# Kernel optimization log

Hardware: AMD Instinct MI355X
Metric: run time of the kernel (lower is better)

## Reference

```python
import jax, jax.numpy as jnp
import numpy as np

TOPK = 3
RAT_S = 0.05


def conv4d(x, w, bs):
    """Faithful fused version of the looped Conv4d (stride=1, padding=1, l_k=3).

    x:  (b, c_in, l, d, h, w)
    w:  (c_out, c_in, l_k, d_k, h_k, w_k)  -- w[:, :, i] is the i-th Conv3d weight
    bs: (l_k, c_out)                        -- per-i Conv3d biases
    The torch loop computes out[f] = sum_i conv3d_i(x[f + i - l_k//2]) for valid
    frame indices, which is exactly a 4D cross-correlation; the bias of conv3d_i
    is added once per VALID i, so boundary frames get fewer bias terms.
    """
    out = jax.lax.conv_general_dilated(
        x, w, window_strides=(1, 1, 1, 1), padding=[(1, 1)] * 4,
        dimension_numbers=("NCABXY", "OIABXY", "NCABXY"))
    l_i = x.shape[2]
    l_k = w.shape[2]
    f = jnp.arange(l_i)
    j = f[:, None] + jnp.arange(l_k)[None, :] - l_k // 2  # source frame per (f, i)
    valid = ((j >= 0) & (j < l_i)).astype(x.dtype)        # (l, l_k)
    bias = valid @ bs                                     # (l, c_out)
    return out + bias.T[None, :, :, None, None, None]


def zero_window(x_aff, h, w, rat_s):
    """x_aff: (b, h*w, h, w). Suppress a Gaussian window centered at each
    channel's (r, c) source location."""
    dt = x_aff.dtype
    sr = jnp.asarray(h * rat_s, dt)
    sc = jnp.asarray(w * rat_s, dt)
    ind_r = jnp.arange(h, dtype=dt)
    ind_c = jnp.arange(w, dtype=dt)
    cent_r = jnp.repeat(jnp.arange(h), w).astype(dt)  # (h*w,)
    cent_c = jnp.tile(jnp.arange(w), h).astype(dt)    # (h*w,)
    gr = jnp.exp(-((ind_r[None, :] - cent_r[:, None]) ** 2) / (2 * sr ** 2))  # (hw, h)
    gc = jnp.exp(-((ind_c[None, :] - cent_c[:, None]) ** 2) / (2 * sc ** 2))  # (hw, w)
    g = 1.0 - gr[:, :, None] * gc[:, None, :]  # (hw, h, w)
    return x_aff * g[None]


def setup_inputs() -> dict:
    key = jax.random.key(0)
    k = jax.random.split(key, 5)
    b, c, h, w = 4, 256, 32, 32
    x = jax.random.normal(k[0], (b, c, h, w), dtype=jnp.float32)
    w1 = jax.random.normal(k[1], (16, 1, 3, 3, 3, 3), dtype=jnp.float32) * 0.2
    b1 = jax.random.normal(k[2], (3, 16), dtype=jnp.float32) * 0.05
    w2 = jax.random.normal(k[3], (1, 16, 3, 3, 3, 3), dtype=jnp.float32) * 0.1
    b2 = jax.random.normal(k[4], (3, 1), dtype=jnp.float32) * 0.05
    return {"x": x, "w1": w1, "b1": b1, "w2": w2, "b2": b2}


def reference(x, w1, b1, w2, b2):
    b, c, h1, ww1 = x.shape
    n = h1 * ww1
    # F.normalize over channel dim (p=2, eps=1e-12)
    xn = x / jnp.maximum(jnp.linalg.norm(x, axis=1, keepdims=True), 1e-12)
    q = xn.transpose(0, 2, 3, 1).reshape(b, n, c)      # (b, hw, c)
    kmat = xn.reshape(b, c, n)                          # (b, c, hw)
    aff = jnp.einsum("bnc,bcm->bnm", q, kmat)          # (b, hw, hw)
    aff = zero_window(aff.reshape(b, n, h1, ww1), h1, ww1, RAT_S)
    x_fc = aff.reshape(b, 1, h1, ww1, h1, ww1)
    y = conv4d(x_fc, w1, b1)                            # (b, 16, h1, w1, h2, w2)
    y = conv4d(y, w2, b2)                               # (b, 1,  h1, w1, h2, w2)
    xc = y.reshape(b, n, h1, ww1)                       # (b, hw, h2, w2)
    # top-k values along dim=-3 (the query/channel axis)
    vals = jax.lax.top_k(xc.transpose(0, 2, 3, 1), TOPK)[0]  # (b, h2, w2, k)
    return vals.transpose(0, 3, 1, 2)                   # (b, k, h2, w2)
```

## Files before the change

kernel.cpp:

```cpp
#include <hip/hip_runtime.h>

#define HW 1024
#define CCH 256


typedef _Float16 h2v __attribute__((ext_vector_type(2)));
typedef short bf16x8 __attribute__((ext_vector_type(8)));
typedef float f32x4 __attribute__((ext_vector_type(4)));

__device__ __forceinline__ float fdot2(unsigned a, unsigned b, float c) {
#if __has_builtin(__builtin_amdgcn_fdot2)
    return __builtin_amdgcn_fdot2(__builtin_bit_cast(h2v, a),
                                  __builtin_bit_cast(h2v, b), c, false);
#else
    h2v ha = __builtin_bit_cast(h2v, a), hb = __builtin_bit_cast(h2v, b);
    return c + (float)ha.x * (float)hb.x + (float)ha.y * (float)hb.y;
#endif
}
__device__ __forceinline__ unsigned packh2(float x, float y) {
    h2v h;
    h.x = (_Float16)x;
    h.y = (_Float16)y;
    return __builtin_bit_cast(unsigned, h);
}
__device__ __forceinline__ unsigned short f2bf(float f) {
    unsigned u = __float_as_uint(f);
    u += 0x7fffu + ((u >> 16) & 1u);
    return (unsigned short)(u >> 16);
}

__global__ __launch_bounds__(256) void norm_kernel(const float* __restrict__ x,
                                                   unsigned short* __restrict__ xnT) {
    __shared__ float red[16][17];
    __shared__ float invs[16];
    int b = blockIdx.y;
    int p0 = blockIdx.x * 16;
    int cg = threadIdx.x >> 4;
    int pp = threadIdx.x & 15;
    int p = p0 + pp;
    const float* xb = x + (size_t)b * CCH * HW;
    float ss = 0.f;
#pragma unroll
    for (int i = 0; i < 16; ++i) {
        float v = xb[(size_t)(cg * 16 + i) * HW + p];
        ss += v * v;
    }
    red[cg][pp] = ss;
    __syncthreads();
    if (threadIdx.x < 16) {
        float s = 0.f;
#pragma unroll
        for (int g = 0; g < 16; ++g) s += red[g][threadIdx.x];
        invs[threadIdx.x] = 1.0f / fmaxf(sqrtf(s), 1e-12f);
    }
    __syncthreads();
    float inv = invs[pp];
    unsigned* o = (unsigned*)(xnT + ((size_t)b * HW + p) * CCH) + cg * 8;
#pragma unroll
    for (int i = 0; i < 8; ++i) {
        int c = cg * 16 + 2 * i;
        unsigned lo = f2bf(xb[(size_t)c * HW + p] * inv);
        unsigned hi = f2bf(xb[(size_t)(c + 1) * HW + p] * inv);
        o[i] = lo | (hi << 16);
    }
}

__global__ __launch_bounds__(256) void aff_kernel(const unsigned short* __restrict__ xnT,
                                                  unsigned short* __restrict__ Af16) {
    int b = blockIdx.z;
    int p0 = blockIdx.y * 64, m0 = blockIdx.x * 64;
    const unsigned short* X = xnT + (size_t)b * HW * CCH;
    int lane = threadIdx.x & 63, w = threadIdx.x >> 6;
    int pw = p0 + (w >> 1) * 32, mw = m0 + (w & 1) * 32;
    int lr = lane & 15, lg = lane >> 4;
    f32x4 acc[2][2] = {};
    for (int ks = 0; ks < 8; ++ks) {
        int kc = ks * 32 + lg * 8;
        bf16x8 a0 = *(const bf16x8*)&X[(size_t)(pw + lr) * CCH + kc];
        bf16x8 a1 = *(const bf16x8*)&X[(size_t)(pw + 16 + lr) * CCH + kc];
        bf16x8 b0 = *(const bf16x8*)&X[(size_t)(mw + lr) * CCH + kc];
        bf16x8 b1 = *(const bf16x8*)&X[(size_t)(mw + 16 + lr) * CCH + kc];
        acc[0][0] = __builtin_amdgcn_mfma_f32_16x16x32_bf16(a0, b0, acc[0][0], 0, 0, 0);
        acc[0][1] = __builtin_amdgcn_mfma_f32_16x16x32_bf16(a0, b1, acc[0][1], 0, 0, 0);
        acc[1][0] = __builtin_amdgcn_mfma_f32_16x16x32_bf16(a1, b0, acc[1][0], 0, 0, 0);
        acc[1][1] = __builtin_amdgcn_mfma_f32_16x16x32_bf16(a1, b1, acc[1][1], 0, 0, 0);
    }
#pragma unroll
    for (int pi = 0; pi < 2; ++pi)
#pragma unroll
        for (int mi = 0; mi < 2; ++mi)
#pragma unroll
            for (int r = 0; r < 4; ++r) {
                int p = pw + 16 * pi + lg * 4 + r;
                int m = mw + 16 * mi + lr;
                int dr = (m >> 5) - (p >> 5);
                int dc = (m & 31) - (p & 31);
                float gg = 1.0f - __expf(-(float)(dr * dr + dc * dc) * 0.1953125f);
                float v = acc[pi][mi][r] * gg;
                Af16[((size_t)b * HW + p) * HW + m] =
                    __builtin_bit_cast(unsigned short, (_Float16)v);
            }
}

__global__ __launch_bounds__(256) void g_kernel(const float* __restrict__ w1,
                                                const float* __restrict__ w2,
                                                float* __restrict__ G) {
    __shared__ float w1s[1296], w2s[1296];
    int tid = threadIdx.x;
    for (int i = tid; i < 1296; i += 256) { w1s[i] = w1[i]; w2s[i] = w2[i]; }
    __syncthreads();
    int idx = blockIdx.x * 256 + tid;
    if (idx < 6561) {
        int o1 = idx / 81, o2 = idx - o1 * 81;
        float s = 0.f;
#pragma unroll
        for (int ch = 0; ch < 16; ++ch) s += w1s[ch * 81 + o1] * w2s[ch * 81 + o2];
        G[idx] = s;
    }
}

__global__ __launch_bounds__(128) void wcomp_kernel(const float* __restrict__ G,
                                                    unsigned* __restrict__ Wpk) {
    __shared__ float Gs[6561];
    int cls = blockIdx.x;
    int t = threadIdx.x;
    for (int i = t; i < 6561; i += 128) Gs[i] = G[i];
    if (t < 25) Wpk[cls * 400 + t * 16 + 15] = 0u;
    __syncthreads();
    if (t >= 125) return;
    int a = t / 25, b_ = (t / 5) % 5, c = t % 5;
    int r1c = cls / 27, c1c = (cls / 9) % 3, r2c = (cls / 3) % 3, c2c = cls % 3;
    float W[5] = {};
    for (int i2 = 0; i2 < 3; ++i2) {
        if ((r1c == 0 && i2 == 0) || (r1c == 2 && i2 == 2)) continue;
        int i1 = a - i2;
        if (i1 < 0 || i1 > 2) continue;
        for (int j2 = 0; j2 < 3; ++j2) {
            if ((c1c == 0 && j2 == 0) || (c1c == 2 && j2 == 2)) continue;
            int j1 = b_ - j2;
            if (j1 < 0 || j1 > 2) continue;
            for (int u2 = 0; u2 < 3; ++u2) {
                if ((r2c == 0 && u2 == 0) || (r2c == 2 && u2 == 2)) continue;
                int u1 = c - u2;
                if (u1 < 0 || u1 > 2) continue;
                for (int v2 = 0; v2 < 3; ++v2) {
                    if ((c2c == 0 && v2 == 0) || (c2c == 2 && v2 == 2)) continue;
                    int o2 = i2 * 27 + j2 * 9 + u2 * 3 + v2;
                    int o1b = i1 * 27 + j1 * 9 + u1 * 3;
#pragma unroll
                    for (int d = 0; d < 5; ++d) {
                        int v1 = d - v2;
                        if (v1 < 0 || v1 > 2) continue;
                        W[d] += Gs[(o1b + v1) * 81 + o2];
                    }
                }
            }
        }
    }
    unsigned* o = &Wpk[cls * 400 + (a * 5 + b_) * 16 + c * 3];
    o[0] = packh2(W[0], W[1]);
    o[1] = packh2(W[2], W[3]);
    o[2] = packh2(W[4], 0.f);
}

__global__ __launch_bounds__(1024) void bt_kernel(const float* __restrict__ w2,
                                                  const float* __restrict__ b1,
                                                  const float* __restrict__ b2,
                                                  float* __restrict__ BT) {
    __shared__ float w2s[1296], b1s[48], S0[81], S1[81], S2[81];
    int t = threadIdx.x;
    for (int i = t; i < 1296; i += 1024) w2s[i] = w2[i];
    if (t < 48) b1s[t] = b1[t];
    __syncthreads();
    if (t < 81) {
        float s0 = 0.f, s1 = 0.f, s2 = 0.f;
#pragma unroll
        for (int ch = 0; ch < 16; ++ch) {
            float w = w2s[ch * 81 + t];
            s0 += w * b1s[16 + ch];
            s1 += w * b1s[ch];
            s2 += w * b1s[32 + ch];
        }
        S0[t] = s0; S1[t] = s1; S2[t] = s2;
    }
    __syncthreads();
    if (t >= 864) return;
    int r1 = t / 27, c1c = (t / 9) % 3, r2c = (t / 3) % 3, c2c = t % 3;
    float s = b2[1] + (r1 >= 1 ? b2[0] : 0.f) + (r1 <= 30 ? b2[2] : 0.f);
    for (int i2 = 0; i2 < 3; ++i2) {
        int rr = r1 + i2 - 1;
        if (rr < 0 || rr > 31) continue;
        float m1 = (rr >= 1) ? 1.f : 0.f, m2 = (rr <= 30) ? 1.f : 0.f;
        for (int j2 = 0; j2 < 3; ++j2) {
            if ((c1c == 0 && j2 == 0) || (c1c == 2 && j2 == 2)) continue;
            for (int u2 = 0; u2 < 3; ++u2) {
                if ((r2c == 0 && u2 == 0) || (r2c == 2 && u2 == 2)) continue;
                for (int v2 = 0; v2 < 3; ++v2) {
                    if ((c2c == 0 && v2 == 0) || (c2c == 2 && v2 == 2)) continue;
                    int o2 = i2 * 27 + j2 * 9 + u2 * 3 + v2;
                    s += S0[o2] + m1 * S1[o2] + m2 * S2[o2];
                }
            }
        }
    }
    BT[t] = s;
}

#define HSD 66
__global__ __launch_bounds__(256) void convc_kernel(const unsigned short* __restrict__ Af16,
                                                    const unsigned* __restrict__ Wpk,
                                                    const float* __restrict__ BT,
                                                    float* __restrict__ xc) {
    __shared__ unsigned halo[4][36 * HSD];
    int tid = threadIdx.x;
    int w = tid >> 6, lane = tid & 63;
    int P = blockIdx.x * 4 + w;
    int b = blockIdx.y;
    int r1 = P >> 5, c1 = P & 31;
    int r1c = (r1 == 0) ? 0 : (r1 == 31) ? 2 : 1;
    int c1c = (c1 == 0) ? 0 : (c1 == 31) ? 2 : 1;

    const uint4* wsrc = (const uint4*)(Wpk + (size_t)((r1c * 3 + c1c) * 9 + 4) * 400);
    float bias = BT[r1 * 27 + c1c * 9 + 4];

    unsigned* myh = halo[w];
    for (int i = lane; i < 36 * HSD; i += 64) myh[i] = 0;

    int qr2 = lane & 15, qc = lane >> 4;
    int srow = lane & 31, sth = lane >> 5;
    int wbase = (srow + 2) * HSD + 8 * sth + 1;
    int idx4 = srow * 4 + sth * 2;

    const uint4* Ab4 = (const uint4*)(Af16 + (size_t)b * HW * HW);

    float acc0[8] = {}, acc1[8] = {};

    int pr0 = min(max(r1 - 2, 0), 31), pc0 = min(max(c1 - 2, 0), 31);
    uint4 pfA = Ab4[(size_t)(pr0 * 32 + pc0) * 128 + idx4];
    uint4 pfB = Ab4[(size_t)(pr0 * 32 + pc0) * 128 + idx4 + 1];

#pragma unroll 1
    for (int tp = 0; tp < 25; ++tp) {
        int tr = tp / 5, tc = tp - tr * 5;
        int apr = r1 + tr - 2, apc = c1 + tc - 2;
        bool valid = ((unsigned)apr < 32u) && ((unsigned)apc < 32u);
        uint4 curA = pfA, curB = pfB;
        if (tp < 24) {
            int t2 = tp + 1;
            int tr2 = t2 / 5, tc2 = t2 - tr2 * 5;
            int npr = min(max(r1 + tr2 - 2, 0), 31);
            int npc = min(max(c1 + tc2 - 2, 0), 31);
            pfA = Ab4[(size_t)(npr * 32 + npc) * 128 + idx4];
            pfB = Ab4[(size_t)(npr * 32 + npc) * 128 + idx4 + 1];
        }

        uint4 w4a = wsrc[tp * 4 + 0];
        uint4 w4b = wsrc[tp * 4 + 1];
        uint4 w4c = wsrc[tp * 4 + 2];
        uint4 w4d = wsrc[tp * 4 + 3];

        __syncthreads();
        if (valid) {
            unsigned* hb = &myh[wbase];
            hb[0] = curA.x; hb[1] = curA.y; hb[2] = curA.z; hb[3] = curA.w;
            hb[4] = curB.x; hb[5] = curB.y; hb[6] = curB.z; hb[7] = curB.w;
        }
        __syncthreads();
        if (!valid) continue;

        unsigned wr[16] = {w4a.x, w4a.y, w4a.z, w4a.w, w4b.x, w4b.y, w4b.z, w4b.w,
                           w4c.x, w4c.y, w4c.z, w4c.w, w4d.x, w4d.y, w4d.z, w4d.w};
        const unsigned* base = &myh[(2 * qr2) * HSD + 4 * qc];
#pragma unroll
        for (int i = 0; i < 6; ++i) {
            const unsigned* rp = base + i * HSD;
            uint2 e0 = *(const uint2*)rp;
            uint2 e1 = *(const uint2*)(rp + 2);
            uint2 e2 = *(const uint2*)(rp + 4);
            unsigned q0 = e0.x, q1 = e0.y, q2 = e1.x, q3 = e1.y, q4 = e2.x, q5 = e2.y;
            unsigned pp[12];
            pp[0] = q0;  pp[2] = q1;  pp[4] = q2;  pp[6] = q3;  pp[8] = q4;  pp[10] = q5;
            pp[1] = (q0 >> 16) | (q1 << 16);
            pp[3] = (q1 >> 16) | (q2 << 16);
            pp[5] = (q2 >> 16) | (q3 << 16);
            pp[7] = (q3 >> 16) | (q4 << 16);
            pp[9] = (q4 >> 16) | (q5 << 16);
            pp[11] = (q5 >> 16);
            if (i <= 4) {
                unsigned wa = wr[i * 3], wb_ = wr[i * 3 + 1], wc_ = wr[i * 3 + 2];
#pragma unroll
                for (int cc = 0; cc < 8; ++cc) {
                    float a = acc0[cc];
                    a = fdot2(wa, pp[cc], a);
                    a = fdot2(wb_, pp[cc + 2], a);
                    a = fdot2(wc_, pp[cc + 4], a);
                    acc0[cc] = a;
                }
            }
            if (i >= 1) {
                int u = i - 1;
                unsigned wa = wr[u * 3], wb_ = wr[u * 3 + 1], wc_ = wr[u * 3 + 2];
#pragma unroll
                for (int cc = 0; cc < 8; ++cc) {
                    float a = acc1[cc];
                    a = fdot2(wa, pp[cc], a);
                    a = fdot2(wb_, pp[cc + 2], a);
                    a = fdot2(wc_, pp[cc + 4], a);
                    acc1[cc] = a;
                }
            }
        }
    }

    float* xp = &xc[((size_t)b * HW + P) * HW];
    int o0 = (2 * qr2) * 32 + 8 * qc;
    int o1 = (2 * qr2 + 1) * 32 + 8 * qc;
    *(float4*)&xp[o0] = make_float4(acc0[0] + bias, acc0[1] + bias, acc0[2] + bias, acc0[3] + bias);
    *(float4*)&xp[o0 + 4] = make_float4(acc0[4] + bias, acc0[5] + bias, acc0[6] + bias, acc0[7] + bias);
    *(float4*)&xp[o1] = make_float4(acc1[0] + bias, acc1[1] + bias, acc1[2] + bias, acc1[3] + bias);
    *(float4*)&xp[o1 + 4] = make_float4(acc1[4] + bias, acc1[5] + bias, acc1[6] + bias, acc1[7] + bias);
}

__global__ __launch_bounds__(256) void expand_kernel(const unsigned short* __restrict__ Af16,
                                                     unsigned* __restrict__ Apad32) {
    int plane = blockIdx.x, b = blockIdx.y;
    const unsigned* src = (const unsigned*)(Af16 + ((size_t)b * HW + plane) * HW);
    unsigned* dst = Apad32 + ((size_t)b * HW + plane) * 720;
    for (int k = threadIdx.x; k < 720; k += 256) {
        int pr = k / 20, pcd = k - pr * 20;
        unsigned val = 0;
        if (pr >= 2 && pr < 34 && pcd >= 1 && pcd <= 16)
            val = src[(pr - 2) * 16 + (pcd - 1)];
        dst[k] = val;
    }
}

__global__ __launch_bounds__(128) void fix_kernel(const unsigned* __restrict__ Apad32,
                                                  const unsigned* __restrict__ Wpk,
                                                  const float* __restrict__ BT,
                                                  float* __restrict__ xc) {
    __shared__ __align__(16) unsigned wl[3600];
    __shared__ float bts[9];
    int tid = threadIdx.x;
    int P = blockIdx.x, b = blockIdx.y;
    int r1 = P >> 5, c1 = P & 31;
    int r1c = (r1 == 0) ? 0 : (r1 == 31) ? 2 : 1;
    int c1c = (c1 == 0) ? 0 : (c1 == 31) ? 2 : 1;

    const unsigned* wsrc = Wpk + (size_t)(r1c * 3 + c1c) * 3600;
    for (int i = tid; i < 3600; i += 128) wl[i] = wsrc[i];
    if (tid < 9) bts[tid] = BT[r1 * 27 + c1c * 9 + tid];

    int li = tid;
    bool act = li < 124;
    int qr, qc;
    if (li < 32) { qr = 0; qc = li; }
    else if (li < 64) { qr = 31; qc = li - 32; }
    else if (li < 94) { qr = li - 63; qc = 0; }
    else { qr = min(li, 123) - 93; qc = 31; }
    int r2c = (qr == 0) ? 0 : (qr == 31) ? 2 : 1;
    int c2c = (qc == 0) ? 0 : (qc == 31) ? 2 : 1;
    int v = r2c * 3 + c2c;
    int sh = (qc & 1) * 16;
    int sd = qc >> 1;

    __syncthreads();
    float acc = 0.f;

#pragma unroll 1
    for (int tp = 0; tp < 25; ++tp) {
        int tr = tp / 5, tc = tp - tr * 5;
        int apr = r1 + tr - 2, apc = c1 + tc - 2;
        if ((unsigned)apr >= 32u || (unsigned)apc >= 32u) continue;
        const unsigned* tpl = Apad32 + ((size_t)b * HW + apr * 32 + apc) * 720;
        const uint4* wv4 = (const uint4*)&wl[v * 400 + tp * 16];
        uint4 wa = wv4[0], wb = wv4[1], wc2 = wv4[2], wd = wv4[3];
        unsigned wr[16] = {wa.x, wa.y, wa.z, wa.w, wb.x, wb.y, wb.z, wb.w,
                           wc2.x, wc2.y, wc2.z, wc2.w, wd.x, wd.y, wd.z, wd.w};
#pragma unroll
        for (int u = 0; u < 5; ++u) {
            const unsigned* rp = tpl + (qr + u) * 20 + sd;
            unsigned d0 = rp[0], d1 = rp[1], d2 = rp[2];
            unsigned pa = __builtin_amdgcn_alignbit(d1, d0, sh);
            unsigned pb = __builtin_amdgcn_alignbit(d2, d1, sh);
            unsigned pc_ = __builtin_amdgcn_alignbit(0u, d2, sh);
            acc = fdot2(wr[u * 3 + 0], pa, acc);
            acc = fdot2(wr[u * 3 + 1], pb, acc);
            acc = fdot2(wr[u * 3 + 2], pc_, acc);
        }
    }

    if (act)
        xc[((size_t)b * HW + P) * HW + qr * 32 + qc] = acc + bts[v];
}

__device__ __forceinline__ void top3_push(float v, float& t0, float& t1, float& t2) {
    float n0 = fminf(t0, v);
    t0 = fmaxf(t0, v);
    float n1 = fminf(t1, n0);
    t1 = fmaxf(t1, n0);
    t2 = fmaxf(t2, n1);
}

__global__ __launch_bounds__(256) void topk1_kernel(const float* __restrict__ xc,
                                                    float* __restrict__ part) {
    int q = blockIdx.x * 256 + threadIdx.x;
    int pc = blockIdx.y, bi = blockIdx.z;
    float t0 = -1e30f, t1 = -1e30f, t2 = -1e30f;
    const float* xp = xc + (size_t)bi * HW * HW;
    for (int p = pc * 32; p < pc * 32 + 32; ++p)
        top3_push(xp[(size_t)p * HW + q], t0, t1, t2);
    float* pp = part + (size_t)(bi * 32 + pc) * 3 * HW;
    pp[q] = t0;
    pp[HW + q] = t1;
    pp[2 * HW + q] = t2;
}

__global__ __launch_bounds__(256) void topk2_kernel(const float* __restrict__ part,
                                                    float* __restrict__ out) {
    int q = blockIdx.x * 256 + threadIdx.x;
    int bi = blockIdx.y;
    float t0 = -1e30f, t1 = -1e30f, t2 = -1e30f;
    const float* pp = part + (size_t)bi * 96 * HW;
    for (int k = 0; k < 96; ++k) top3_push(pp[(size_t)k * HW + q], t0, t1, t2);
    float* ob = out + (size_t)bi * 3 * HW;
    ob[q] = t0;
    ob[HW + q] = t1;
    ob[2 * HW + q] = t2;
}

extern "C" void kernel_launch(void* const* d_in, const int* in_sizes, int n_in,
                              void* d_out, int out_size, void* d_ws, size_t ws_size,
                              hipStream_t stream) {
    const float* x = (const float*)d_in[0];
    const float* w1 = (const float*)d_in[1];
    const float* b1 = (const float*)d_in[2];
    const float* w2 = (const float*)d_in[3];
    const float* b2 = (const float*)d_in[4];
    float* out = (float*)d_out;
    float* ws = (float*)d_ws;

    unsigned short* xnT = (unsigned short*)ws;
    unsigned short* Af16 = (unsigned short*)(ws + 524288);
    float* xc = ws + 2621440;
    unsigned* Wpk = (unsigned*)(ws + 6815744);
    float* BT = ws + 6848512;
    float* part = ws + 6849536;
    unsigned* Apad32 = (unsigned*)(ws + 7242752);
    float* G = ws + 10191872;

    norm_kernel<<<dim3(64, 4), 256, 0, stream>>>(x, xnT);
    aff_kernel<<<dim3(16, 16, 4), 256, 0, stream>>>(xnT, Af16);
    expand_kernel<<<dim3(1024, 4), 256, 0, stream>>>(Af16, Apad32);
    g_kernel<<<26, 256, 0, stream>>>(w1, w2, G);
    wcomp_kernel<<<81, 128, 0, stream>>>(G, Wpk);
    bt_kernel<<<1, 1024, 0, stream>>>(w2, b1, b2, BT);
    convc_kernel<<<dim3(256, 4), 256, 0, stream>>>(Af16, Wpk, BT, xc);
    fix_kernel<<<dim3(1024, 4), 128, 0, stream>>>(Apad32, Wpk, BT, xc);
    topk1_kernel<<<dim3(4, 32, 4), 256, 0, stream>>>(xc, part);
    topk2_kernel<<<dim3(4, 4), 256, 0, stream>>>(part, out);
}
```

Baseline: 175.1 us.

## Fuse padded-affinity expansion into aff kernel and G computation into wcomp

The aff kernel now also writes each fp16 affinity value straight into the zero-padded plane layout that fix_kernel reads, so the separate expand kernel and its full re-read of Af16 go away. The padding is zeroed up front with a memset. The g_kernel is folded into wcomp_kernel, which recomputes the weight-product matrix in shared memory per block, saving a launch and a global round trip. convc's halo row stride shrinks from 66 to 34 and a minimum-occupancy launch bound is added. In exchange, aff's extra stores are scattered 2-byte writes, the memset adds a full-buffer write, and every wcomp block repeats the G computation.

```diff
diff --git a/kernel.cpp b/kernel.cpp
--- a/kernel.cpp
+++ b/kernel.cpp
@@ -66,7 +66,8 @@
 }
 
 __global__ __launch_bounds__(256) void aff_kernel(const unsigned short* __restrict__ xnT,
-                                                  unsigned short* __restrict__ Af16) {
+                                                  unsigned short* __restrict__ Af16,
+                                                  unsigned short* __restrict__ Apad16) {
     int b = blockIdx.z;
     int p0 = blockIdx.y * 64, m0 = blockIdx.x * 64;
     const unsigned short* X = xnT + (size_t)b * HW * CCH;
@@ -97,35 +98,29 @@
                 int dc = (m & 31) - (p & 31);
                 float gg = 1.0f - __expf(-(float)(dr * dr + dc * dc) * 0.1953125f);
                 float v = acc[pi][mi][r] * gg;
-                Af16[((size_t)b * HW + p) * HW + m] =
-                    __builtin_bit_cast(unsigned short, (_Float16)v);
+                unsigned short hv = __builtin_bit_cast(unsigned short, (_Float16)v);
+                Af16[((size_t)b * HW + p) * HW + m] = hv;
+                Apad16[(((size_t)b * HW + p) * 36 + 2 + (m >> 5)) * 40 + 2 + (m & 31)] = hv;
             }
 }
 
-__global__ __launch_bounds__(256) void g_kernel(const float* __restrict__ w1,
-                                                const float* __restrict__ w2,
-                                                float* __restrict__ G) {
-    __shared__ float w1s[1296], w2s[1296];
-    int tid = threadIdx.x;
-    for (int i = tid; i < 1296; i += 256) { w1s[i] = w1[i]; w2s[i] = w2[i]; }
-    __syncthreads();
-    int idx = blockIdx.x * 256 + tid;
-    if (idx < 6561) {
-        int o1 = idx / 81, o2 = idx - o1 * 81;
-        float s = 0.f;
-#pragma unroll
-        for (int ch = 0; ch < 16; ++ch) s += w1s[ch * 81 + o1] * w2s[ch * 81 + o2];
-        G[idx] = s;
-    }
-}
-
-__global__ __launch_bounds__(128) void wcomp_kernel(const float* __restrict__ G,
+__global__ __launch_bounds__(128) void wcomp_kernel(const float* __restrict__ w1,
+                                                    const float* __restrict__ w2,
                                                     unsigned* __restrict__ Wpk) {
     __shared__ float Gs[6561];
+    __shared__ float w1s[1296], w2s[1296];
     int cls = blockIdx.x;
     int t = threadIdx.x;
-    for (int i = t; i < 6561; i += 128) Gs[i] = G[i];
+    for (int i = t; i < 1296; i += 128) { w1s[i] = w1[i]; w2s[i] = w2[i]; }
     if (t < 25) Wpk[cls * 400 + t * 16 + 15] = 0u;
+    __syncthreads();
+    for (int i = t; i < 6561; i += 128) {
+        int o1 = i / 81, o2 = i - o1 * 81;
+        float s = 0.f;
+#pragma unroll
+        for (int ch = 0; ch < 16; ++ch) s += w1s[ch * 81 + o1] * w2s[ch * 81 + o2];
+        Gs[i] = s;
+    }
     __syncthreads();
     if (t >= 125) return;
     int a = t / 25, b_ = (t / 5) % 5, c = t % 5;
@@ -206,11 +201,11 @@
     BT[t] = s;
 }
 
-#define HSD 66
-__global__ __launch_bounds__(256) void convc_kernel(const unsigned short* __restrict__ Af16,
-                                                    const unsigned* __restrict__ Wpk,
-                                                    const float* __restrict__ BT,
-                                                    float* __restrict__ xc) {
+#define HSD 34
+__global__ __launch_bounds__(256, 8) void convc_kernel(const unsigned short* __restrict__ Af16,
+                                                       const unsigned* __restrict__ Wpk,
+                                                       const float* __restrict__ BT,
+                                                       float* __restrict__ xc) {
     __shared__ unsigned halo[4][36 * HSD];
     int tid = threadIdx.x;
     int w = tid >> 6, lane = tid & 63;
@@ -321,20 +316,6 @@
     *(float4*)&xp[o1 + 4] = make_float4(acc1[4] + bias, acc1[5] + bias, acc1[6] + bias, acc1[7] + bias);
 }
 
-__global__ __launch_bounds__(256) void expand_kernel(const unsigned short* __restrict__ Af16,
-                                                     unsigned* __restrict__ Apad32) {
-    int plane = blockIdx.x, b = blockIdx.y;
-    const unsigned* src = (const unsigned*)(Af16 + ((size_t)b * HW + plane) * HW);
-    unsigned* dst = Apad32 + ((size_t)b * HW + plane) * 720;
-    for (int k = threadIdx.x; k < 720; k += 256) {
-        int pr = k / 20, pcd = k - pr * 20;
-        unsigned val = 0;
-        if (pr >= 2 && pr < 34 && pcd >= 1 && pcd <= 16)
-            val = src[(pr - 2) * 16 + (pcd - 1)];
-        dst[k] = val;
-    }
-}
-
 __global__ __launch_bounds__(128) void fix_kernel(const unsigned* __restrict__ Apad32,
                                                   const unsigned* __restrict__ Wpk,
                                                   const float* __restrict__ BT,
@@ -447,13 +428,11 @@
     float* BT = ws + 6848512;
     float* part = ws + 6849536;
     unsigned* Apad32 = (unsigned*)(ws + 7242752);
-    float* G = ws + 10191872;
-
+
+    hipMemsetAsync(Apad32, 0, (size_t)4 * 1024 * 36 * 40 * 2, stream);
     norm_kernel<<<dim3(64, 4), 256, 0, stream>>>(x, xnT);
-    aff_kernel<<<dim3(16, 16, 4), 256, 0, stream>>>(xnT, Af16);
-    expand_kernel<<<dim3(1024, 4), 256, 0, stream>>>(Af16, Apad32);
-    g_kernel<<<26, 256, 0, stream>>>(w1, w2, G);
-    wcomp_kernel<<<81, 128, 0, stream>>>(G, Wpk);
+    aff_kernel<<<dim3(16, 16, 4), 256, 0, stream>>>(xnT, Af16, (unsigned short*)Apad32);
+    wcomp_kernel<<<81, 128, 0, stream>>>(w1, w2, Wpk);
     bt_kernel<<<1, 1024, 0, stream>>>(w2, b1, b2, BT);
     convc_kernel<<<dim3(256, 4), 256, 0, stream>>>(Af16, Wpk, BT, xc);
     fix_kernel<<<dim3(1024, 4), 128, 0, stream>>>(Apad32, Wpk, BT, xc);
```

Result: slower. 185.0 us (+5.7%).

## Split convc planes across two waves, fuse G into wcomp, stage fix tiles in LDS

Applied to the files above, without the earlier changes.

The center-region conv kernel now gives each affinity plane to two waves, each computing half the output rows with 4 columns per lane. This halves per-wave accumulators and LDS halo size and doubles the grid, with launch bounds asking for higher occupancy. The G weight-product kernel is folded into wcomp, removing one launch and a global round trip. fix_kernel now copies each padded plane into shared memory before the boundary-lane dot products, at the cost of extra barriers per tap.

```diff
diff --git a/kernel.cpp b/kernel.cpp
--- a/kernel.cpp
+++ b/kernel.cpp
@@ -102,30 +102,37 @@
             }
 }
 
-__global__ __launch_bounds__(256) void g_kernel(const float* __restrict__ w1,
-                                                const float* __restrict__ w2,
-                                                float* __restrict__ G) {
-    __shared__ float w1s[1296], w2s[1296];
-    int tid = threadIdx.x;
-    for (int i = tid; i < 1296; i += 256) { w1s[i] = w1[i]; w2s[i] = w2[i]; }
-    __syncthreads();
-    int idx = blockIdx.x * 256 + tid;
-    if (idx < 6561) {
-        int o1 = idx / 81, o2 = idx - o1 * 81;
-        float s = 0.f;
-#pragma unroll
-        for (int ch = 0; ch < 16; ++ch) s += w1s[ch * 81 + o1] * w2s[ch * 81 + o2];
-        G[idx] = s;
-    }
-}
-
-__global__ __launch_bounds__(128) void wcomp_kernel(const float* __restrict__ G,
+__global__ __launch_bounds__(256) void expand_kernel(const unsigned short* __restrict__ Af16,
+                                                     unsigned* __restrict__ Apad32) {
+    int plane = blockIdx.x, b = blockIdx.y;
+    const unsigned* src = (const unsigned*)(Af16 + ((size_t)b * HW + plane) * HW);
+    unsigned* dst = Apad32 + ((size_t)b * HW + plane) * 720;
+    for (int k = threadIdx.x; k < 720; k += 256) {
+        int pr = k / 20, pcd = k - pr * 20;
+        unsigned val = 0;
+        if (pr >= 2 && pr < 34 && pcd >= 1 && pcd <= 16)
+            val = src[(pr - 2) * 16 + (pcd - 1)];
+        dst[k] = val;
+    }
+}
+
+__global__ __launch_bounds__(128) void wcomp_kernel(const float* __restrict__ w1,
+                                                    const float* __restrict__ w2,
                                                     unsigned* __restrict__ Wpk) {
     __shared__ float Gs[6561];
+    __shared__ float w1s[1296], w2s[1296];
     int cls = blockIdx.x;
     int t = threadIdx.x;
-    for (int i = t; i < 6561; i += 128) Gs[i] = G[i];
+    for (int i = t; i < 1296; i += 128) { w1s[i] = w1[i]; w2s[i] = w2[i]; }
     if (t < 25) Wpk[cls * 400 + t * 16 + 15] = 0u;
+    __syncthreads();
+    for (int i = t; i < 6561; i += 128) {
+        int o1 = i / 81, o2 = i - o1 * 81;
+        float s = 0.f;
+#pragma unroll
+        for (int ch = 0; ch < 16; ++ch) s += w1s[ch * 81 + o1] * w2s[ch * 81 + o2];
+        Gs[i] = s;
+    }
     __syncthreads();
     if (t >= 125) return;
     int a = t / 25, b_ = (t / 5) % 5, c = t % 5;
@@ -206,15 +213,16 @@
     BT[t] = s;
 }
 
-#define HSD 66
-__global__ __launch_bounds__(256) void convc_kernel(const unsigned short* __restrict__ Af16,
-                                                    const unsigned* __restrict__ Wpk,
-                                                    const float* __restrict__ BT,
-                                                    float* __restrict__ xc) {
-    __shared__ unsigned halo[4][36 * HSD];
+#define HSD 34
+__global__ __launch_bounds__(256, 8) void convc_kernel(const unsigned short* __restrict__ Af16,
+                                                       const unsigned* __restrict__ Wpk,
+                                                       const float* __restrict__ BT,
+                                                       float* __restrict__ xc) {
+    __shared__ unsigned halo[2][36 * HSD];
     int tid = threadIdx.x;
     int w = tid >> 6, lane = tid & 63;
-    int P = blockIdx.x * 4 + w;
+    int pl = w >> 1, h = w & 1;
+    int P = blockIdx.x * 2 + pl;
     int b = blockIdx.y;
     int r1 = P >> 5, c1 = P & 31;
     int r1c = (r1 == 0) ? 0 : (r1 == 31) ? 2 : 1;
@@ -223,35 +231,35 @@
     const uint4* wsrc = (const uint4*)(Wpk + (size_t)((r1c * 3 + c1c) * 9 + 4) * 400);
     float bias = BT[r1 * 27 + c1c * 9 + 4];
 
-    unsigned* myh = halo[w];
-    for (int i = lane; i < 36 * HSD; i += 64) myh[i] = 0;
-
-    int qr2 = lane & 15, qc = lane >> 4;
-    int srow = lane & 31, sth = lane >> 5;
-    int wbase = (srow + 2) * HSD + 8 * sth + 1;
-    int idx4 = srow * 4 + sth * 2;
+    for (int i = tid; i < 2 * 36 * HSD; i += 256) ((unsigned*)halo)[i] = 0;
+    unsigned* myh = halo[pl];
+
+    int qr2 = 8 * h + (lane & 7);
+    int qc = lane >> 3;
+    int srow = lane & 31;
+    int sth2 = 2 * h + (lane >> 5);
+    int wbase = (srow + 2) * HSD + 4 * sth2 + 1;
+    int idx4 = srow * 4 + sth2;
 
     const uint4* Ab4 = (const uint4*)(Af16 + (size_t)b * HW * HW);
 
-    float acc0[8] = {}, acc1[8] = {};
+    float acc0[4] = {}, acc1[4] = {};
 
     int pr0 = min(max(r1 - 2, 0), 31), pc0 = min(max(c1 - 2, 0), 31);
-    uint4 pfA = Ab4[(size_t)(pr0 * 32 + pc0) * 128 + idx4];
-    uint4 pfB = Ab4[(size_t)(pr0 * 32 + pc0) * 128 + idx4 + 1];
+    uint4 pf = Ab4[(size_t)(pr0 * 32 + pc0) * 128 + idx4];
 
 #pragma unroll 1
     for (int tp = 0; tp < 25; ++tp) {
         int tr = tp / 5, tc = tp - tr * 5;
         int apr = r1 + tr - 2, apc = c1 + tc - 2;
         bool valid = ((unsigned)apr < 32u) && ((unsigned)apc < 32u);
-        uint4 curA = pfA, curB = pfB;
+        uint4 cur = pf;
         if (tp < 24) {
             int t2 = tp + 1;
             int tr2 = t2 / 5, tc2 = t2 - tr2 * 5;
             int npr = min(max(r1 + tr2 - 2, 0), 31);
             int npc = min(max(c1 + tc2 - 2, 0), 31);
-            pfA = Ab4[(size_t)(npr * 32 + npc) * 128 + idx4];
-            pfB = Ab4[(size_t)(npr * 32 + npc) * 128 + idx4 + 1];
+            pf = Ab4[(size_t)(npr * 32 + npc) * 128 + idx4];
         }
 
         uint4 w4a = wsrc[tp * 4 + 0];
@@ -262,77 +270,57 @@
         __syncthreads();
         if (valid) {
             unsigned* hb = &myh[wbase];
-            hb[0] = curA.x; hb[1] = curA.y; hb[2] = curA.z; hb[3] = curA.w;
-            hb[4] = curB.x; hb[5] = curB.y; hb[6] = curB.z; hb[7] = curB.w;
+            hb[0] = cur.x; hb[1] = cur.y; hb[2] = cur.z; hb[3] = cur.w;
         }
         __syncthreads();
         if (!valid) continue;
 
         unsigned wr[16] = {w4a.x, w4a.y, w4a.z, w4a.w, w4b.x, w4b.y, w4b.z, w4b.w,
                            w4c.x, w4c.y, w4c.z, w4c.w, w4d.x, w4d.y, w4d.z, w4d.w};
-        const unsigned* base = &myh[(2 * qr2) * HSD + 4 * qc];
+        const unsigned* base = &myh[(2 * qr2) * HSD + 2 * qc];
 #pragma unroll
         for (int i = 0; i < 6; ++i) {
             const unsigned* rp = base + i * HSD;
             uint2 e0 = *(const uint2*)rp;
             uint2 e1 = *(const uint2*)(rp + 2);
-            uint2 e2 = *(const uint2*)(rp + 4);
-            unsigned q0 = e0.x, q1 = e0.y, q2 = e1.x, q3 = e1.y, q4 = e2.x, q5 = e2.y;
-            unsigned pp[12];
-            pp[0] = q0;  pp[2] = q1;  pp[4] = q2;  pp[6] = q3;  pp[8] = q4;  pp[10] = q5;
+            unsigned q0 = e0.x, q1 = e0.y, q2 = e1.x, q3 = e1.y;
+            unsigned pp[8];
+            pp[0] = q0; pp[2] = q1; pp[4] = q2; pp[6] = q3;
             pp[1] = (q0 >> 16) | (q1 << 16);
             pp[3] = (q1 >> 16) | (q2 << 16);
             pp[5] = (q2 >> 16) | (q3 << 16);
-            pp[7] = (q3 >> 16) | (q4 << 16);
-            pp[9] = (q4 >> 16) | (q5 << 16);
-            pp[11] = (q5 >> 16);
+            pp[7] = (q3 >> 16);
             if (i <= 4) {
                 unsigned wa = wr[i * 3], wb_ = wr[i * 3 + 1], wc_ = wr[i * 3 + 2];
 #pragma unroll
-                for (int cc = 0; cc < 8; ++cc) {
-                    float a = acc0[cc];
-                    a = fdot2(wa, pp[cc], a);
-                    a = fdot2(wb_, pp[cc + 2], a);
-                    a = fdot2(wc_, pp[cc + 4], a);
-                    acc0[cc] = a;
+                for (int j = 0; j < 4; ++j) {
+                    float a = acc0[j];
+                    a = fdot2(wa, pp[j], a);
+                    a = fdot2(wb_, pp[j + 2], a);
+                    a = fdot2(wc_, pp[j + 4], a);
+                    acc0[j] = a;
                 }
             }
             if (i >= 1) {
                 int u = i - 1;
                 unsigned wa = wr[u * 3], wb_ = wr[u * 3 + 1], wc_ = wr[u * 3 + 2];
 #pragma unroll
-                for (int cc = 0; cc < 8; ++cc) {
-                    float a = acc1[cc];
-                    a = fdot2(wa, pp[cc], a);
-                    a = fdot2(wb_, pp[cc + 2], a);
-                    a = fdot2(wc_, pp[cc + 4], a);
-                    acc1[cc] = a;
+                for (int j = 0; j < 4; ++j) {
+                    float a = acc1[j];
+                    a = fdot2(wa, pp[j], a);
+                    a = fdot2(wb_, pp[j + 2], a);
+                    a = fdot2(wc_, pp[j + 4], a);
+                    acc1[j] = a;
                 }
             }
         }
     }
 
     float* xp = &xc[((size_t)b * HW + P) * HW];
-    int o0 = (2 * qr2) * 32 + 8 * qc;
-    int o1 = (2 * qr2 + 1) * 32 + 8 * qc;
+    int o0 = (2 * qr2) * 32 + 4 * qc;
+    int o1 = (2 * qr2 + 1) * 32 + 4 * qc;
     *(float4*)&xp[o0] = make_float4(acc0[0] + bias, acc0[1] + bias, acc0[2] + bias, acc0[3] + bias);
-    *(float4*)&xp[o0 + 4] = make_float4(acc0[4] + bias, acc0[5] + bias, acc0[6] + bias, acc0[7] + bias);
     *(float4*)&xp[o1] = make_float4(acc1[0] + bias, acc1[1] + bias, acc1[2] + bias, acc1[3] + bias);
-    *(float4*)&xp[o1 + 4] = make_float4(acc1[4] + bias, acc1[5] + bias, acc1[6] + bias, acc1[7] + bias);
-}
-
-__global__ __launch_bounds__(256) void expand_kernel(const unsigned short* __restrict__ Af16,
-                                                     unsigned* __restrict__ Apad32) {
-    int plane = blockIdx.x, b = blockIdx.y;
-    const unsigned* src = (const unsigned*)(Af16 + ((size_t)b * HW + plane) * HW);
-    unsigned* dst = Apad32 + ((size_t)b * HW + plane) * 720;
-    for (int k = threadIdx.x; k < 720; k += 256) {
-        int pr = k / 20, pcd = k - pr * 20;
-        unsigned val = 0;
-        if (pr >= 2 && pr < 34 && pcd >= 1 && pcd <= 16)
-            val = src[(pr - 2) * 16 + (pcd - 1)];
-        dst[k] = val;
-    }
 }
 
 __global__ __launch_bounds__(128) void fix_kernel(const unsigned* __restrict__ Apad32,
@@ -340,6 +328,7 @@
                                                   const float* __restrict__ BT,
                                                   float* __restrict__ xc) {
     __shared__ __align__(16) unsigned wl[3600];
+    __shared__ unsigned plb[720];
     __shared__ float bts[9];
     int tid = threadIdx.x;
     int P = blockIdx.x, b = blockIdx.y;
@@ -364,7 +353,6 @@
     int sh = (qc & 1) * 16;
     int sd = qc >> 1;
 
-    __syncthreads();
     float acc = 0.f;
 
 #pragma unroll 1
@@ -373,20 +361,25 @@
         int apr = r1 + tr - 2, apc = c1 + tc - 2;
         if ((unsigned)apr >= 32u || (unsigned)apc >= 32u) continue;
         const unsigned* tpl = Apad32 + ((size_t)b * HW + apr * 32 + apc) * 720;
+        __syncthreads();
+        for (int i = tid; i < 720; i += 128) plb[i] = tpl[i];
+        __syncthreads();
         const uint4* wv4 = (const uint4*)&wl[v * 400 + tp * 16];
         uint4 wa = wv4[0], wb = wv4[1], wc2 = wv4[2], wd = wv4[3];
         unsigned wr[16] = {wa.x, wa.y, wa.z, wa.w, wb.x, wb.y, wb.z, wb.w,
                            wc2.x, wc2.y, wc2.z, wc2.w, wd.x, wd.y, wd.z, wd.w};
-#pragma unroll
-        for (int u = 0; u < 5; ++u) {
-            const unsigned* rp = tpl + (qr + u) * 20 + sd;
-            unsigned d0 = rp[0], d1 = rp[1], d2 = rp[2];
-            unsigned pa = __builtin_amdgcn_alignbit(d1, d0, sh);
-            unsigned pb = __builtin_amdgcn_alignbit(d2, d1, sh);
-            unsigned pc_ = __builtin_amdgcn_alignbit(0u, d2, sh);
-            acc = fdot2(wr[u * 3 + 0], pa, acc);
-            acc = fdot2(wr[u * 3 + 1], pb, acc);
-            acc = fdot2(wr[u * 3 + 2], pc_, acc);
+        if (act) {
+#pragma unroll
+            for (int u = 0; u < 5; ++u) {
+                const unsigned* rp = &plb[(qr + u) * 20 + sd];
+                unsigned d0 = rp[0], d1 = rp[1], d2 = rp[2];
+                unsigned pa = __builtin_amdgcn_alignbit(d1, d0, sh);
+                unsigned pb = __builtin_amdgcn_alignbit(d2, d1, sh);
+                unsigned pc_ = __builtin_amdgcn_alignbit(0u, d2, sh);
+                acc = fdot2(wr[u * 3 + 0], pa, acc);
+                acc = fdot2(wr[u * 3 + 1], pb, acc);
+                acc = fdot2(wr[u * 3 + 2], pc_, acc);
+            }
         }
     }
 
@@ -447,15 +440,13 @@
     float* BT = ws + 6848512;
     float* part = ws + 6849536;
     unsigned* Apad32 = (unsigned*)(ws + 7242752);
-    float* G = ws + 10191872;
 
     norm_kernel<<<dim3(64, 4), 256, 0, stream>>>(x, xnT);
     aff_kernel<<<dim3(16, 16, 4), 256, 0, stream>>>(xnT, Af16);
     expand_kernel<<<dim3(1024, 4), 256, 0, stream>>>(Af16, Apad32);
-    g_kernel<<<26, 256, 0, stream>>>(w1, w2, G);
-    wcomp_kernel<<<81, 128, 0, stream>>>(G, Wpk);
+    wcomp_kernel<<<81, 128, 0, stream>>>(w1, w2, Wpk);
     bt_kernel<<<1, 1024, 0, stream>>>(w2, b1, b2, BT);
-    convc_kernel<<<dim3(256, 4), 256, 0, stream>>>(Af16, Wpk, BT, xc);
+    convc_kernel<<<dim3(512, 4), 256, 0, stream>>>(Af16, Wpk, BT, xc);
     fix_kernel<<<dim3(1024, 4), 128, 0, stream>>>(Apad32, Wpk, BT, xc);
     topk1_kernel<<<dim3(4, 32, 4), 256, 0, stream>>>(xc, part);
     topk2_kernel<<<dim3(4, 4), 256, 0, stream>>>(part, out);
```

Measured after the change: 233.2 us. 1.33x slower.
